# Kernel tuning notes

Measured on AMD Instinct MI355X. Metric: run time of the kernel, lower is better.

## Reference

```python
import jax, jax.numpy as jnp
import numpy as np

N = 100000   # nodes
E = 1600000  # edges
F = 128      # n_feat
HID = 64     # n_hid
L = 4        # n_layer
C = 40       # n_class
TEMP = 0.1   # summarize temperature


def setup_inputs() -> dict:
    key = jax.random.key(0)
    ks = jax.random.split(key, 10)
    x = jax.random.normal(ks[0], (N, F), dtype=jnp.float32)
    edge_index = jax.random.randint(ks[1], (2, E), 0, N, dtype=jnp.int64)
    s_in = 1.0 / np.sqrt(F)
    s_h = 1.0 / np.sqrt(HID)
    W0 = jax.random.normal(ks[2], (F, HID), dtype=jnp.float32) * s_in
    b0 = jnp.zeros((HID,), dtype=jnp.float32)
    Ws = jax.random.normal(ks[3], (L - 1, HID, HID), dtype=jnp.float32) * s_h
    bs = jnp.zeros((L - 1, HID), dtype=jnp.float32)
    Wq = jax.random.normal(ks[4], (HID, HID), dtype=jnp.float32) * s_h
    Wk = jax.random.normal(ks[5], (HID, HID), dtype=jnp.float32) * s_h
    Wout = jax.random.normal(ks[6], (HID, C), dtype=jnp.float32) * s_h
    bout = jnp.zeros((C,), dtype=jnp.float32)
    return {"x": x, "edge_index": edge_index, "W0": W0, "b0": b0,
            "Ws": Ws, "bs": bs, "Wq": Wq, "Wk": Wk, "Wout": Wout, "bout": bout}


def reference(x, edge_index, W0, b0, Ws, bs, Wq, Wk, Wout, bout):
    # --- GCN normalization with self-loops (symmetric D^-1/2 (A+I) D^-1/2) ---
    loop = jnp.arange(N, dtype=edge_index.dtype)
    src = jnp.concatenate([edge_index[0], loop])  # [E+N]
    dst = jnp.concatenate([edge_index[1], loop])
    deg = jax.ops.segment_sum(jnp.ones_like(dst, dtype=x.dtype), dst, num_segments=N)
    dinv = jnp.where(deg > 0, jax.lax.rsqrt(deg), 0.0)
    enorm = dinv[src] * dinv[dst]  # [E+N]

    def propagate(h):
        # gather -> scale -> scatter-add (sparse matvec)
        msg = h[src] * enorm[:, None]
        return jax.ops.segment_sum(msg, dst, num_segments=N)

    # --- twin-branch stacked GCN convs (x_ starts as detached copy; eval mode => no dropout) ---
    h, h_ = x, x
    hs, hs_ = [], []
    for l in range(L):
        W = W0 if l == 0 else Ws[l - 1]
        b = b0 if l == 0 else bs[l - 1]
        h = jax.nn.relu(propagate(h @ W) + b)
        h_ = jax.nn.relu(propagate(h_ @ W) + b)
        hs.append(h)
        hs_.append(h_)

    Hm = jnp.stack(hs)    # [L, N, HID]
    Hm_ = jnp.stack(hs_)  # [L, N, HID]

    # --- Summarize: per-node attention over layer scales; query from twin branch ---
    q = jnp.einsum('lnd,de->lne', Hm_, Wq)
    k = jnp.einsum('lnd,de->lne', Hm, Wk)
    scores = jnp.sum(q * k, axis=-1) / TEMP      # [L, N]
    att = jax.nn.softmax(scores, axis=0)         # softmax over layers
    hsum = jnp.einsum('ln,lnd->nd', att, Hm)     # [N, HID]

    return hsum @ Wout + bout                    # [N, C]
```

## Files before the change

### kernel.cpp

```cpp
#include <hip/hip_runtime.h>
#include <hip/hip_bf16.h>
#include <math.h>

#define NN 100000
#define EE 1600000
#define FF 128
#define HH 64
#define CC 40

constexpr int SCAN_B = 1024;
constexpr int NB = (NN + SCAN_B - 1) / SCAN_B;

constexpr int RN = NN / 8;
constexpr int FB = 128;
constexpr int CHUNK = EE / FB;
constexpr int SELFB = (RN + FB - 1) / FB;

__global__ void k_init_deg(int* __restrict__ deg) {
    int i = blockIdx.x * 256 + threadIdx.x;
    if (i < NN) deg[i] = 1;
}

__global__ void k_count(const int* __restrict__ ei, int* __restrict__ deg) {
    const int g = blockIdx.x & 7;
    const int j = blockIdx.x >> 3;
    const int lo = g * RN, hi = lo + RN;
    const int* __restrict__ dstp = ei + EE;
    const int e1 = (j + 1) * CHUNK;
    for (int e = j * CHUNK + threadIdx.x; e < e1; e += 256) {
        int d = dstp[e];
        if (d >= lo && d < hi) atomicAdd(&deg[d], 1);
    }
}

__global__ void k_dinv(const int* __restrict__ deg, float* __restrict__ dinv) {
    int i = blockIdx.x * 256 + threadIdx.x;
    if (i < NN) dinv[i] = rsqrtf((float)deg[i]);
}

__global__ void k_scanA(const int* __restrict__ deg, int* __restrict__ excl, int* __restrict__ bsum) {
    __shared__ int s[SCAN_B];
    int t = threadIdx.x;
    int g = blockIdx.x * SCAN_B + t;
    int v = (g < NN) ? deg[g] : 0;
    s[t] = v;
    __syncthreads();
    for (int o = 1; o < SCAN_B; o <<= 1) {
        int u = (t >= o) ? s[t - o] : 0;
        __syncthreads();
        s[t] += u;
        __syncthreads();
    }
    if (g < NN) excl[g] = s[t] - v;
    if (t == SCAN_B - 1) bsum[blockIdx.x] = s[t];
}

__global__ void k_scanB(int* __restrict__ bsum) {
    __shared__ int s[128];
    int t = threadIdx.x;
    int v = (t < NB) ? bsum[t] : 0;
    s[t] = v;
    __syncthreads();
    for (int o = 1; o < 128; o <<= 1) {
        int u = (t >= o) ? s[t - o] : 0;
        __syncthreads();
        s[t] += u;
        __syncthreads();
    }
    if (t < NB) bsum[t] = s[t] - v;
}

__global__ void k_scanC(int* __restrict__ rp, const int* __restrict__ bsum, int* __restrict__ cursor) {
    int t = threadIdx.x;
    int g = blockIdx.x * SCAN_B + t;
    if (g < NN) {
        int v = rp[g] + bsum[blockIdx.x];
        rp[g] = v;
        cursor[g] = v;
    }
    if (g == 0) rp[NN] = EE + NN;
}

__global__ void k_fill(const int* __restrict__ ei, int* __restrict__ cursor, int* __restrict__ cs) {
    const int g = blockIdx.x & 7;
    const int j = blockIdx.x >> 3;
    const int lo = g * RN, hi = lo + RN;
    const int* __restrict__ dstp = ei + EE;
    const int e1 = (j + 1) * CHUNK;
    for (int e = j * CHUNK + threadIdx.x; e < e1; e += 256) {
        int d = dstp[e];
        if (d >= lo && d < hi) {
            int s = ei[e];
            int p = atomicAdd(&cursor[d], 1);
            cs[p] = s;
        }
    }
    int n = lo + j * SELFB + threadIdx.x;
    if (threadIdx.x < SELFB && n < hi) {
        int p = atomicAdd(&cursor[n], 1);
        cs[p] = n;
    }
}

template <int K>
__global__ __launch_bounds__(256) void k_gemm(const float* __restrict__ A, const float* __restrict__ W,
                                              const float* __restrict__ dinv, float* __restrict__ Z,
                                              int nrows) {
    constexpr int S = 68;
    __shared__ float wl[64 * 64];
    __shared__ float hl[64 * S];
    const int t = threadIdx.x;
    const int r0 = blockIdx.x * 64;
    const int rg = t >> 4, cg = t & 15;
    float acc[4][4] = {};

    for (int kb = 0; kb < K; kb += 64) {
        {
            const float4* Wv = (const float4*)(W + kb * 64);
            for (int i = t; i < 1024; i += 256) ((float4*)wl)[i] = Wv[i];
        }
        for (int i = t; i < 1024; i += 256) {
            int row = i >> 4, d4 = i & 15;
            float4 v = {0.f, 0.f, 0.f, 0.f};
            if (r0 + row < nrows) v = *(const float4*)(A + (size_t)(r0 + row) * K + kb + d4 * 4);
            *(float4*)(hl + row * S + d4 * 4) = v;
        }
        __syncthreads();
#pragma unroll 8
        for (int d = 0; d < 64; ++d) {
            float4 w4 = *(const float4*)(wl + d * 64 + cg * 4);
#pragma unroll
            for (int i = 0; i < 4; i++) {
                float h = hl[(rg * 4 + i) * S + d];
                acc[i][0] = fmaf(h, w4.x, acc[i][0]);
                acc[i][1] = fmaf(h, w4.y, acc[i][1]);
                acc[i][2] = fmaf(h, w4.z, acc[i][2]);
                acc[i][3] = fmaf(h, w4.w, acc[i][3]);
            }
        }
        __syncthreads();
    }
#pragma unroll
    for (int i = 0; i < 4; i++) {
        int row = r0 + rg * 4 + i;
        if (row < nrows) {
            float dv = dinv[row];
            float4 o = {acc[i][0] * dv, acc[i][1] * dv, acc[i][2] * dv, acc[i][3] * dv};
            *(float4*)(Z + (size_t)row * 64 + cg * 4) = o;
        }
    }
}

__global__ __launch_bounds__(256) void k_prepM(const float* __restrict__ Wq, const float* __restrict__ Wk,
                                               float* __restrict__ M) {
    __shared__ float wk[64 * 65];
    __shared__ float wq[4 * 64];
    const int t = threadIdx.x;
    for (int i = t; i < 1024; i += 256) {
        int r = i >> 4, c4 = i & 15;
        float4 v = ((const float4*)Wk)[i];
        wk[r * 65 + c4 * 4 + 0] = v.x;
        wk[r * 65 + c4 * 4 + 1] = v.y;
        wk[r * 65 + c4 * 4 + 2] = v.z;
        wk[r * 65 + c4 * 4 + 3] = v.w;
    }
    const int rbase = blockIdx.x * 4;
    wq[t] = Wq[rbase * 64 + t];
    __syncthreads();
    const int rr = t >> 6;
    const int c = t & 63;
    float acc = 0.f;
#pragma unroll 8
    for (int e = 0; e < 64; ++e) acc = fmaf(wq[rr * 64 + e], wk[c * 65 + e], acc);
    M[(rbase + rr) * 64 + c] = acc;
}

__global__ __launch_bounds__(256) void k_score(const float* __restrict__ Hm, const float* __restrict__ M,
                                               float* __restrict__ scores) {
    constexpr int S = 68;
    __shared__ float wl[4096];
    __shared__ float hl[64 * S];
    const int t = threadIdx.x;
    const int r0 = blockIdx.x * 64;
    for (int i = t; i < 1024; i += 256) ((float4*)wl)[i] = ((const float4*)M)[i];
    for (int i = t; i < 1024; i += 256) {
        int row = i >> 4, d4 = i & 15;
        *(float4*)(hl + row * S + d4 * 4) = *(const float4*)(Hm + (size_t)(r0 + row) * 64 + d4 * 4);
    }
    __syncthreads();
    const int rg = t >> 4, cg = t & 15;
    float u[4][4] = {};
#pragma unroll 8
    for (int d = 0; d < 64; ++d) {
        float4 m4 = *(const float4*)(wl + d * 64 + cg * 4);
#pragma unroll
        for (int i = 0; i < 4; i++) {
            float h = hl[(rg * 4 + i) * S + d];
            u[i][0] = fmaf(h, m4.x, u[i][0]);
            u[i][1] = fmaf(h, m4.y, u[i][1]);
            u[i][2] = fmaf(h, m4.z, u[i][2]);
            u[i][3] = fmaf(h, m4.w, u[i][3]);
        }
    }
#pragma unroll
    for (int i = 0; i < 4; i++) {
        const float* hrow = hl + (rg * 4 + i) * S + cg * 4;
        float p = u[i][0] * hrow[0] + u[i][1] * hrow[1] + u[i][2] * hrow[2] + u[i][3] * hrow[3];
        p += __shfl_xor(p, 1);
        p += __shfl_xor(p, 2);
        p += __shfl_xor(p, 4);
        p += __shfl_xor(p, 8);
        if (cg == 0) scores[r0 + rg * 4 + i] = p;
    }
}

__global__ __launch_bounds__(256) void k_prop(const float* __restrict__ z, const int* __restrict__ rp,
                                              const int* __restrict__ cs, const float* __restrict__ dinv,
                                              const float* __restrict__ bias, float* __restrict__ out) {
    const int lane = threadIdx.x & 63;
    const int g = lane >> 4;
    const int l4 = lane & 15;
    const int n = blockIdx.x * 16 + (threadIdx.x >> 6) * 4 + g;
    const int beg = rp[n], end = rp[n + 1];
    float4 a0 = {0, 0, 0, 0}, a1 = {0, 0, 0, 0}, a2 = {0, 0, 0, 0}, a3 = {0, 0, 0, 0};
    int i = beg;
    for (; i + 8 <= end; i += 8) {
        int c0 = __builtin_nontemporal_load(cs + i);
        int c1 = __builtin_nontemporal_load(cs + i + 1);
        int c2 = __builtin_nontemporal_load(cs + i + 2);
        int c3 = __builtin_nontemporal_load(cs + i + 3);
        int c4 = __builtin_nontemporal_load(cs + i + 4);
        int c5 = __builtin_nontemporal_load(cs + i + 5);
        int c6 = __builtin_nontemporal_load(cs + i + 6);
        int c7 = __builtin_nontemporal_load(cs + i + 7);
        float4 z0 = *(const float4*)(z + (size_t)(unsigned)c0 * 64 + l4 * 4);
        float4 z1 = *(const float4*)(z + (size_t)(unsigned)c1 * 64 + l4 * 4);
        float4 z2 = *(const float4*)(z + (size_t)(unsigned)c2 * 64 + l4 * 4);
        float4 z3 = *(const float4*)(z + (size_t)(unsigned)c3 * 64 + l4 * 4);
        float4 z4 = *(const float4*)(z + (size_t)(unsigned)c4 * 64 + l4 * 4);
        float4 z5 = *(const float4*)(z + (size_t)(unsigned)c5 * 64 + l4 * 4);
        float4 z6 = *(const float4*)(z + (size_t)(unsigned)c6 * 64 + l4 * 4);
        float4 z7 = *(const float4*)(z + (size_t)(unsigned)c7 * 64 + l4 * 4);
        a0.x += z0.x; a0.y += z0.y; a0.z += z0.z; a0.w += z0.w;
        a1.x += z1.x; a1.y += z1.y; a1.z += z1.z; a1.w += z1.w;
        a2.x += z2.x; a2.y += z2.y; a2.z += z2.z; a2.w += z2.w;
        a3.x += z3.x; a3.y += z3.y; a3.z += z3.z; a3.w += z3.w;
        a0.x += z4.x; a0.y += z4.y; a0.z += z4.z; a0.w += z4.w;
        a1.x += z5.x; a1.y += z5.y; a1.z += z5.z; a1.w += z5.w;
        a2.x += z6.x; a2.y += z6.y; a2.z += z6.z; a2.w += z6.w;
        a3.x += z7.x; a3.y += z7.y; a3.z += z7.z; a3.w += z7.w;
    }
    for (; i + 4 <= end; i += 4) {
        int c0 = __builtin_nontemporal_load(cs + i);
        int c1 = __builtin_nontemporal_load(cs + i + 1);
        int c2 = __builtin_nontemporal_load(cs + i + 2);
        int c3 = __builtin_nontemporal_load(cs + i + 3);
        float4 z0 = *(const float4*)(z + (size_t)(unsigned)c0 * 64 + l4 * 4);
        float4 z1 = *(const float4*)(z + (size_t)(unsigned)c1 * 64 + l4 * 4);
        float4 z2 = *(const float4*)(z + (size_t)(unsigned)c2 * 64 + l4 * 4);
        float4 z3 = *(const float4*)(z + (size_t)(unsigned)c3 * 64 + l4 * 4);
        a0.x += z0.x; a0.y += z0.y; a0.z += z0.z; a0.w += z0.w;
        a1.x += z1.x; a1.y += z1.y; a1.z += z1.z; a1.w += z1.w;
        a2.x += z2.x; a2.y += z2.y; a2.z += z2.z; a2.w += z2.w;
        a3.x += z3.x; a3.y += z3.y; a3.z += z3.z; a3.w += z3.w;
    }
    for (; i < end; ++i) {
        int c = __builtin_nontemporal_load(cs + i);
        float4 zr = *(const float4*)(z + (size_t)(unsigned)c * 64 + l4 * 4);
        a0.x += zr.x; a0.y += zr.y; a0.z += zr.z; a0.w += zr.w;
    }
    const float dn = dinv[n];
    const float4 b4 = *(const float4*)(bias + l4 * 4);
    float4 r;
    r.x = fmaf(dn, (a0.x + a1.x) + (a2.x + a3.x), b4.x);
    r.y = fmaf(dn, (a0.y + a1.y) + (a2.y + a3.y), b4.y);
    r.z = fmaf(dn, (a0.z + a1.z) + (a2.z + a3.z), b4.z);
    r.w = fmaf(dn, (a0.w + a1.w) + (a2.w + a3.w), b4.w);
    r.x = r.x > 0.f ? r.x : 0.f;
    r.y = r.y > 0.f ? r.y : 0.f;
    r.z = r.z > 0.f ? r.z : 0.f;
    r.w = r.w > 0.f ? r.w : 0.f;
    *(float4*)(out + (size_t)n * 64 + l4 * 4) = r;
}

__global__ __launch_bounds__(256) void k_sum(const float* __restrict__ Hm, const float* __restrict__ scores,
                                             const float* __restrict__ Wout, const float* __restrict__ bout,
                                             float* __restrict__ out) {
    __shared__ float wo[64 * CC];
    __shared__ float hsl[4][64];
    const int t = threadIdx.x;
    for (int i = t; i < (64 * CC) / 4; i += 256) ((float4*)wo)[i] = ((const float4*)Wout)[i];
    __syncthreads();
    const int lane = t & 63;
    const int wid = t >> 6;
    const int n = blockIdx.x * 4 + wid;
    float h0 = Hm[(size_t)(0 * NN + n) * 64 + lane];
    float h1 = Hm[(size_t)(1 * NN + n) * 64 + lane];
    float h2 = Hm[(size_t)(2 * NN + n) * 64 + lane];
    float h3 = Hm[(size_t)(3 * NN + n) * 64 + lane];
    float s0 = scores[0 * NN + n] * 10.f;
    float s1 = scores[1 * NN + n] * 10.f;
    float s2 = scores[2 * NN + n] * 10.f;
    float s3 = scores[3 * NN + n] * 10.f;
    float m = fmaxf(fmaxf(s0, s1), fmaxf(s2, s3));
    float e0 = __expf(s0 - m), e1 = __expf(s1 - m), e2 = __expf(s2 - m), e3 = __expf(s3 - m);
    float inv = 1.f / (e0 + e1 + e2 + e3);
    float hs = (e0 * h0 + e1 * h1 + e2 * h2 + e3 * h3) * inv;
    hsl[wid][lane] = hs;
    float acc = 0.f;
#pragma unroll 8
    for (int d = 0; d < 64; ++d) {
        if (lane < CC) acc = fmaf(hsl[wid][d], wo[d * CC + lane], acc);
    }
    if (lane < CC) out[(size_t)n * CC + lane] = acc + bout[lane];
}

extern "C" void kernel_launch(void* const* d_in, const int* in_sizes, int n_in,
                              void* d_out, int out_size, void* d_ws, size_t ws_size,
                              hipStream_t stream) {
    const float* x    = (const float*)d_in[0];
    const int*   ei   = (const int*)d_in[1];
    const float* W0   = (const float*)d_in[2];
    const float* b0   = (const float*)d_in[3];
    const float* Ws   = (const float*)d_in[4];
    const float* bs   = (const float*)d_in[5];
    const float* Wq   = (const float*)d_in[6];
    const float* Wk   = (const float*)d_in[7];
    const float* Wout = (const float*)d_in[8];
    const float* bout = (const float*)d_in[9];
    float* out = (float*)d_out;

    char* p = (char*)d_ws;
    auto carve = [&](size_t bytes) {
        void* r = (void*)p;
        p += (bytes + 255) & ~(size_t)255;
        return r;
    };
    int*   deg     = (int*)carve((size_t)NN * 4);
    float* dinv    = (float*)carve((size_t)NN * 4);
    int*   row_ptr = (int*)carve((size_t)(NN + 1) * 4);
    int*   cursor  = (int*)carve((size_t)NN * 4);
    int*   bsum    = (int*)carve(256 * 4);
    int*   cs      = (int*)carve((size_t)(EE + NN) * 4);
    float* M       = (float*)carve((size_t)HH * HH * 4);
    float* z       = (float*)carve((size_t)NN * HH * 4);
    float* Hm      = (float*)carve((size_t)4 * NN * HH * 4);
    float* scores  = (float*)carve((size_t)4 * NN * 4);
    (void)ws_size; (void)n_in; (void)in_sizes; (void)out_size;

    const int GB_N  = (NN + 255) / 256;
    const int GFILL = FB * 8;
    const int GT    = (NN + 63) / 64;
    const int GSC   = (4 * NN) / 64;
    const int GP    = NN / 16;
    const int GS    = NN / 4;

    k_init_deg<<<GB_N, 256, 0, stream>>>(deg);
    k_count<<<GFILL, 256, 0, stream>>>(ei, deg);
    k_dinv<<<GB_N, 256, 0, stream>>>(deg, dinv);
    k_scanA<<<NB, SCAN_B, 0, stream>>>(deg, row_ptr, bsum);
    k_scanB<<<1, 128, 0, stream>>>(bsum);
    k_scanC<<<NB, SCAN_B, 0, stream>>>(row_ptr, bsum, cursor);
    k_fill<<<GFILL, 256, 0, stream>>>(ei, cursor, cs);
    k_prepM<<<16, 256, 0, stream>>>(Wq, Wk, M);

    k_gemm<FF><<<GT, 256, 0, stream>>>(x, W0, dinv, z, NN);
    k_prop<<<GP, 256, 0, stream>>>(z, row_ptr, cs, dinv, b0, Hm);
    for (int l = 1; l < 4; ++l) {
        k_gemm<HH><<<GT, 256, 0, stream>>>(Hm + (size_t)(l - 1) * NN * HH,
                                           Ws + (size_t)(l - 1) * HH * HH, dinv, z, NN);
        k_prop<<<GP, 256, 0, stream>>>(z, row_ptr, cs, dinv, bs + (size_t)(l - 1) * HH,
                                       Hm + (size_t)l * NN * HH);
    }

    k_score<<<GSC, 256, 0, stream>>>(Hm, M, scores);
    k_sum<<<GS, 256, 0, stream>>>(Hm, scores, Wout, bout, out);
}
```

Before: 716.1 us.

## Pre-bucket edges by destination range before degree count and CSR fill

Adds a single pass that partitions edges into 8 destination-range buckets using block-local shared counters and one global atomic per bucket per block. The degree-count and CSR-fill kernels then read only their own bucket instead of each range group rescanning the whole destination array. This removes repeated full reads of the edge list. It adds extra bucket buffers and write traffic, and edges beyond the fixed per-bucket capacity would be silently dropped.

```diff
diff --git a/kernel.cpp b/kernel.cpp
--- a/kernel.cpp
+++ b/kernel.cpp
@@ -12,24 +12,61 @@
 constexpr int NB = (NN + SCAN_B - 1) / SCAN_B;
 
 constexpr int RN = NN / 8;
-constexpr int FB = 128;
-constexpr int CHUNK = EE / FB;
-constexpr int SELFB = (RN + FB - 1) / FB;
-
-__global__ void k_init_deg(int* __restrict__ deg) {
+constexpr int BCAP = 220000;
+constexpr int NE_BLK = 2000;
+constexpr int ABLK = EE / NE_BLK;
+constexpr int GBLK = 64;
+constexpr int SELFB2 = (RN + GBLK - 1) / GBLK;
+
+__global__ void k_init(int* __restrict__ deg, int* __restrict__ bcnt) {
     int i = blockIdx.x * 256 + threadIdx.x;
     if (i < NN) deg[i] = 1;
-}
-
-__global__ void k_count(const int* __restrict__ ei, int* __restrict__ deg) {
+    if (i < 8) bcnt[i] = 0;
+}
+
+__global__ __launch_bounds__(256) void k_bucket(const int* __restrict__ ei, int* __restrict__ bcnt,
+                                                int* __restrict__ bsrc, int* __restrict__ bdst) {
+    __shared__ int lcnt[8], lbase[8], loff[8];
+    const int t = threadIdx.x;
+    if (t < 8) { lcnt[t] = 0; loff[t] = 0; }
+    __syncthreads();
+    const int e0 = blockIdx.x * NE_BLK;
+    int es[8], ed[8];
+    int kmax = 0;
+#pragma unroll
+    for (int k = 0; k < 8; ++k) {
+        int e = e0 + t + k * 256;
+        if (t + k * 256 < NE_BLK) {
+            es[k] = ei[e];
+            ed[k] = ei[EE + e];
+            atomicAdd(&lcnt[ed[k] / RN], 1);
+            kmax = k + 1;
+        }
+    }
+    __syncthreads();
+    if (t < 8) lbase[t] = atomicAdd(&bcnt[t], lcnt[t]);
+    __syncthreads();
+#pragma unroll
+    for (int k = 0; k < 8; ++k) {
+        if (k < kmax) {
+            int b = ed[k] / RN;
+            int pos = lbase[b] + atomicAdd(&loff[b], 1);
+            if (pos < BCAP) {
+                bsrc[b * BCAP + pos] = es[k];
+                bdst[b * BCAP + pos] = ed[k];
+            }
+        }
+    }
+}
+
+__global__ void k_count2(const int* __restrict__ bdst, const int* __restrict__ bcnt,
+                         int* __restrict__ deg) {
     const int g = blockIdx.x & 7;
     const int j = blockIdx.x >> 3;
-    const int lo = g * RN, hi = lo + RN;
-    const int* __restrict__ dstp = ei + EE;
-    const int e1 = (j + 1) * CHUNK;
-    for (int e = j * CHUNK + threadIdx.x; e < e1; e += 256) {
-        int d = dstp[e];
-        if (d >= lo && d < hi) atomicAdd(&deg[d], 1);
+    const int cnt = bcnt[g];
+    const int* __restrict__ dp = bdst + g * BCAP;
+    for (int i = j * 256 + threadIdx.x; i < cnt; i += GBLK * 256) {
+        atomicAdd(&deg[dp[i]], 1);
     }
 }
 
@@ -81,22 +118,21 @@
     if (g == 0) rp[NN] = EE + NN;
 }
 
-__global__ void k_fill(const int* __restrict__ ei, int* __restrict__ cursor, int* __restrict__ cs) {
+__global__ void k_fill2(const int* __restrict__ bsrc, const int* __restrict__ bdst,
+                        const int* __restrict__ bcnt, int* __restrict__ cursor, int* __restrict__ cs) {
     const int g = blockIdx.x & 7;
     const int j = blockIdx.x >> 3;
-    const int lo = g * RN, hi = lo + RN;
-    const int* __restrict__ dstp = ei + EE;
-    const int e1 = (j + 1) * CHUNK;
-    for (int e = j * CHUNK + threadIdx.x; e < e1; e += 256) {
-        int d = dstp[e];
-        if (d >= lo && d < hi) {
-            int s = ei[e];
-            int p = atomicAdd(&cursor[d], 1);
-            cs[p] = s;
-        }
-    }
-    int n = lo + j * SELFB + threadIdx.x;
-    if (threadIdx.x < SELFB && n < hi) {
+    const int cnt = bcnt[g];
+    const int* __restrict__ sp = bsrc + g * BCAP;
+    const int* __restrict__ dp = bdst + g * BCAP;
+    for (int i = j * 256 + threadIdx.x; i < cnt; i += GBLK * 256) {
+        int d = dp[i];
+        int p = atomicAdd(&cursor[d], 1);
+        cs[p] = sp[i];
+    }
+    const int lo = g * RN;
+    int n = lo + j * SELFB2 + threadIdx.x;
+    if (threadIdx.x < SELFB2 && n < lo + RN) {
         int p = atomicAdd(&cursor[n], 1);
         cs[p] = n;
     }
@@ -341,6 +377,9 @@
     int*   row_ptr = (int*)carve((size_t)(NN + 1) * 4);
     int*   cursor  = (int*)carve((size_t)NN * 4);
     int*   bsum    = (int*)carve(256 * 4);
+    int*   bcnt    = (int*)carve(8 * 4);
+    int*   bsrc    = (int*)carve((size_t)8 * BCAP * 4);
+    int*   bdst    = (int*)carve((size_t)8 * BCAP * 4);
     int*   cs      = (int*)carve((size_t)(EE + NN) * 4);
     float* M       = (float*)carve((size_t)HH * HH * 4);
     float* z       = (float*)carve((size_t)NN * HH * 4);
@@ -349,19 +388,19 @@
     (void)ws_size; (void)n_in; (void)in_sizes; (void)out_size;
 
     const int GB_N  = (NN + 255) / 256;
-    const int GFILL = FB * 8;
     const int GT    = (NN + 63) / 64;
     const int GSC   = (4 * NN) / 64;
     const int GP    = NN / 16;
     const int GS    = NN / 4;
 
-    k_init_deg<<<GB_N, 256, 0, stream>>>(deg);
-    k_count<<<GFILL, 256, 0, stream>>>(ei, deg);
+    k_init<<<GB_N, 256, 0, stream>>>(deg, bcnt);
+    k_bucket<<<ABLK, 256, 0, stream>>>(ei, bcnt, bsrc, bdst);
+    k_count2<<<GBLK * 8, 256, 0, stream>>>(bdst, bcnt, deg);
     k_dinv<<<GB_N, 256, 0, stream>>>(deg, dinv);
     k_scanA<<<NB, SCAN_B, 0, stream>>>(deg, row_ptr, bsum);
     k_scanB<<<1, 128, 0, stream>>>(bsum);
     k_scanC<<<NB, SCAN_B, 0, stream>>>(row_ptr, bsum, cursor);
-    k_fill<<<GFILL, 256, 0, stream>>>(ei, cursor, cs);
+    k_fill2<<<GBLK * 8, 256, 0, stream>>>(bsrc, bdst, bcnt, cursor, cs);
     k_prepM<<<16, 256, 0, stream>>>(Wq, Wk, M);
 
     k_gemm<FF><<<GT, 256, 0, stream>>>(x, W0, dinv, z, NN);
```

Result: no change. 720.8 us (+0.7%).
